# Optimization experiments

Hardware: AMD Instinct MI355X
Metric: run time of the kernel (lower is better)

Reference implementation:

```python
import jax, jax.numpy as jnp
import numpy as np

N = 100000   # nodes
E = 1600000  # edges (avg degree 16)
D = 64       # feature dim
STEPS = 3

def setup_inputs() -> dict:
    key = jax.random.key(0)
    ks = jax.random.split(key, 16)
    def rn(i, shape, scale=1.0):
        return jax.random.normal(ks[i], shape, dtype=jnp.float32) * scale
    inp = {
        "nodes": rn(0, (N, D)),
        "edges": rn(1, (E, D)),
        "globals_": rn(2, (1, D)),
        "senders": jax.random.randint(ks[3], (E,), 0, N, dtype=jnp.int32),
        "receivers": jax.random.randint(ks[4], (E,), 0, N, dtype=jnp.int32),
        # edge MLP: in 4*D -> D -> D
        "We1": rn(5, (4 * D, D), (4 * D) ** -0.5),
        "be1": jnp.zeros((D,), jnp.float32),
        "We2": rn(6, (D, D), D ** -0.5),
        "be2": jnp.zeros((D,), jnp.float32),
        # node MLP: in 3*D -> D -> D
        "Wn1": rn(7, (3 * D, D), (3 * D) ** -0.5),
        "bn1": jnp.zeros((D,), jnp.float32),
        "Wn2": rn(8, (D, D), D ** -0.5),
        "bn2": jnp.zeros((D,), jnp.float32),
        # global MLP: in 3*D -> D -> D
        "Wg1": rn(9, (3 * D, D), (3 * D) ** -0.5),
        "bg1": jnp.zeros((D,), jnp.float32),
        "Wg2": rn(10, (D, D), D ** -0.5),
        "bg2": jnp.zeros((D,), jnp.float32),
    }
    return inp

def _mlp(x, W1, b1, W2, b2):
    return jax.nn.relu(x @ W1 + b1) @ W2 + b2

def reference(nodes, edges, globals_, senders, receivers,
              We1, be1, We2, be2, Wn1, bn1, Wn2, bn2, Wg1, bg1, Wg2, bg2):
    g = globals_  # [1, D], single graph
    n_nodes = nodes.shape[0]
    for _ in range(STEPS):
        # --- edge update: gather sender/receiver node feats + broadcast globals ---
        sent = nodes[senders]        # [E, D]
        recv = nodes[receivers]      # [E, D]
        ge = jnp.broadcast_to(g, (edges.shape[0], g.shape[-1]))
        edges = _mlp(jnp.concatenate([edges, sent, recv, ge], axis=-1),
                     We1, be1, We2, be2)  # [E, D]
        # --- aggregate edges to nodes (received messages) ---
        received = jax.ops.segment_sum(edges, receivers, num_segments=n_nodes)
        gn = jnp.broadcast_to(g, (n_nodes, g.shape[-1]))
        nodes = _mlp(jnp.concatenate([nodes, received, gn], axis=-1),
                     Wn1, bn1, Wn2, bn2)  # [N, D]
        # --- aggregate to globals (single graph => full sums) ---
        agg_n = jnp.sum(nodes, axis=0, keepdims=True)  # [1, D]
        agg_e = jnp.sum(edges, axis=0, keepdims=True)  # [1, D]
        g = _mlp(jnp.concatenate([agg_n, agg_e, g], axis=-1),
                 Wg1, bg1, Wg2, bg2)  # [1, D]
    return nodes, edges, g
```

## Files before the change

kernel.cpp:

```cpp
#include <hip/hip_runtime.h>

#define DD 64
typedef unsigned int uint32;
typedef unsigned short ushort16;
typedef short bf16x8 __attribute__((ext_vector_type(8)));
typedef float f32x4 __attribute__((ext_vector_type(4)));
typedef uint32 u32x4 __attribute__((ext_vector_type(4)));

__device__ __forceinline__ ushort16 f2bf(float x) {
    uint32 u = __float_as_uint(x);
    uint32 r = (u + 0x7FFFu + ((u >> 16) & 1u)) >> 16;
    return (ushort16)r;
}
__device__ __forceinline__ float bf2f(ushort16 h) {
    return __uint_as_float(((uint32)h) << 16);
}

__device__ __forceinline__ void split8f(const float4& a, const float4& b, bf16x8& ah, bf16x8& al) {
    float xs[8] = {a.x, a.y, a.z, a.w, b.x, b.y, b.z, b.w};
#pragma unroll
    for (int i = 0; i < 8; ++i) {
        ushort16 hi = f2bf(xs[i]);
        ah[i] = (short)hi;
        al[i] = (short)f2bf(xs[i] - bf2f(hi));
    }
}

__device__ __forceinline__ void mfma_ks(const unsigned short* __restrict__ wks, int l,
                                        const bf16x8* ah, const bf16x8* al, f32x4 (*acc)[4]) {
#pragma unroll
    for (int tt = 0; tt < 4; ++tt) {
        bf16x8 bh = *(const bf16x8*)(wks + ((size_t)(tt * 2 + 0) * 64 + l) * 8);
        bf16x8 bl = *(const bf16x8*)(wks + ((size_t)(tt * 2 + 1) * 64 + l) * 8);
#pragma unroll
        for (int m = 0; m < 4; ++m) {
            acc[m][tt] = __builtin_amdgcn_mfma_f32_16x16x32_bf16(ah[m], bh, acc[m][tt], 0, 0, 0);
            acc[m][tt] = __builtin_amdgcn_mfma_f32_16x16x32_bf16(ah[m], bl, acc[m][tt], 0, 0, 0);
            acc[m][tt] = __builtin_amdgcn_mfma_f32_16x16x32_bf16(al[m], bh, acc[m][tt], 0, 0, 0);
        }
    }
}
__device__ __forceinline__ void mfma_ks_hi(const unsigned short* __restrict__ wks, int l,
                                           const bf16x8* ah, f32x4 (*acc)[4]) {
#pragma unroll
    for (int tt = 0; tt < 4; ++tt) {
        bf16x8 bh = *(const bf16x8*)(wks + ((size_t)(tt * 2 + 0) * 64 + l) * 8);
        bf16x8 bl = *(const bf16x8*)(wks + ((size_t)(tt * 2 + 1) * 64 + l) * 8);
#pragma unroll
        for (int m = 0; m < 4; ++m) {
            acc[m][tt] = __builtin_amdgcn_mfma_f32_16x16x32_bf16(ah[m], bh, acc[m][tt], 0, 0, 0);
            acc[m][tt] = __builtin_amdgcn_mfma_f32_16x16x32_bf16(ah[m], bl, acc[m][tt], 0, 0, 0);
        }
    }
}
__device__ __forceinline__ void mfma_ks1(const unsigned short* __restrict__ wks, int l,
                                         bf16x8 ah, bf16x8 al, f32x4* acc) {
#pragma unroll
    for (int tt = 0; tt < 4; ++tt) {
        bf16x8 bh = *(const bf16x8*)(wks + ((size_t)(tt * 2 + 0) * 64 + l) * 8);
        bf16x8 bl = *(const bf16x8*)(wks + ((size_t)(tt * 2 + 1) * 64 + l) * 8);
        acc[tt] = __builtin_amdgcn_mfma_f32_16x16x32_bf16(ah, bh, acc[tt], 0, 0, 0);
        acc[tt] = __builtin_amdgcn_mfma_f32_16x16x32_bf16(ah, bl, acc[tt], 0, 0, 0);
        acc[tt] = __builtin_amdgcn_mfma_f32_16x16x32_bf16(al, bh, acc[tt], 0, 0, 0);
    }
}
__device__ __forceinline__ void mfma_ks1_hi(const unsigned short* __restrict__ wks, int l,
                                            bf16x8 ah, f32x4* acc) {
#pragma unroll
    for (int tt = 0; tt < 4; ++tt) {
        bf16x8 bh = *(const bf16x8*)(wks + ((size_t)(tt * 2 + 0) * 64 + l) * 8);
        bf16x8 bl = *(const bf16x8*)(wks + ((size_t)(tt * 2 + 1) * 64 + l) * 8);
        acc[tt] = __builtin_amdgcn_mfma_f32_16x16x32_bf16(ah, bh, acc[tt], 0, 0, 0);
        acc[tt] = __builtin_amdgcn_mfma_f32_16x16x32_bf16(ah, bl, acc[tt], 0, 0, 0);
    }
}

__global__ void zero_counts_kernel(int* __restrict__ counts, int N) {
    int i = blockIdx.x * blockDim.x + threadIdx.x;
    if (i < N) counts[i] = 0;
}
__global__ void hist_kernel(const int* __restrict__ idx, int* __restrict__ counts, int E) {
    int i = blockIdx.x * blockDim.x + threadIdx.x;
    if (i < E) atomicAdd(&counts[idx[i]], 1);
}
__global__ __launch_bounds__(1024) void scan_kernel(const int* __restrict__ counts,
                                                    int* __restrict__ offs,
                                                    int* __restrict__ cursor, int N) {
    __shared__ int sm[1024];
    __shared__ int carryS;
    int t = threadIdx.x;
    if (t == 0) carryS = 0;
    __syncthreads();
    for (int base = 0; base < N; base += 4096) {
        int idx = base + t * 4;
        int x0 = (idx + 0 < N) ? counts[idx + 0] : 0;
        int x1 = (idx + 1 < N) ? counts[idx + 1] : 0;
        int x2 = (idx + 2 < N) ? counts[idx + 2] : 0;
        int x3 = (idx + 3 < N) ? counts[idx + 3] : 0;
        int s1 = x0 + x1, s2 = s1 + x2, s3 = s2 + x3;
        sm[t] = s3;
        __syncthreads();
        for (int d = 1; d < 1024; d <<= 1) {
            int v = (t >= d) ? sm[t - d] : 0;
            __syncthreads();
            sm[t] += v;
            __syncthreads();
        }
        int excl = sm[t] - s3 + carryS;
        if (idx < N)     { offs[idx]     = excl;      cursor[idx]     = excl; }
        if (idx + 1 < N) { offs[idx + 1] = excl + x0; cursor[idx + 1] = excl + x0; }
        if (idx + 2 < N) { offs[idx + 2] = excl + s1; cursor[idx + 2] = excl + s1; }
        if (idx + 3 < N) { offs[idx + 3] = excl + s2; cursor[idx + 3] = excl + s2; }
        int chunkTotal = sm[1023];
        __syncthreads();
        if (t == 0) carryS += chunkTotal;
        __syncthreads();
    }
    if (t == 0) offs[N] = carryS;
}
__global__ void scatter_kernel(const int* __restrict__ recv, int* __restrict__ cursor,
                               int* __restrict__ perm, int* __restrict__ inv, int E) {
    int i = blockIdx.x * blockDim.x + threadIdx.x;
    if (i < E) {
        int p = atomicAdd(&cursor[recv[i]], 1);
        perm[p] = i;
        inv[i] = p;
    }
}
__global__ void idxperm_kernel(const int* __restrict__ recv, const int* __restrict__ send,
                               const int* __restrict__ perm,
                               int* __restrict__ ridp, int* __restrict__ sidp, int E) {
    int i = blockIdx.x * blockDim.x + threadIdx.x;
    if (i < E) {
        int pe = perm[i];
        ridp[i] = recv[pe];
        sidp[i] = send[pe];
    }
}

__global__ void prep_bias_kernel(const float* __restrict__ g,
                                 const float* __restrict__ We1, const float* __restrict__ be1,
                                 const float* __restrict__ Wn1, const float* __restrict__ bn1,
                                 float* __restrict__ be1e, float* __restrict__ bn1e) {
    int j = threadIdx.x;
    float a = be1[j];
    float b = bn1[j];
    for (int k = 0; k < DD; ++k) {
        float gk = g[k];
        a = fmaf(gk, We1[(192 + k) * DD + j], a);
        b = fmaf(gk, Wn1[(128 + k) * DD + j], b);
    }
    be1e[j] = a;
    bn1e[j] = b;
}

__global__ void prep_nodes_kernel(const float* __restrict__ src,
                                  unsigned short* __restrict__ h, unsigned short* __restrict__ l,
                                  int total) {
    int i = blockIdx.x * blockDim.x + threadIdx.x;
    if (i < total) {
        float x = src[i];
        ushort16 hi = f2bf(x);
        h[i] = hi;
        l[i] = f2bf(x - bf2f(hi));
    }
}

__global__ void prep_edges_kernel(const float* __restrict__ e0, const int* __restrict__ inv,
                                  unsigned short* __restrict__ ebf, int E) {
    int tid = blockIdx.x * blockDim.x + threadIdx.x;
    if (tid < E * 8) {
        int e = tid >> 3, part = tid & 7;
        const float* p = e0 + (size_t)e * DD + part * 8;
        float4 a = *(const float4*)(p);
        float4 b = *(const float4*)(p + 4);
        u32x4 o;
        o.x = (uint32)f2bf(a.x) | ((uint32)f2bf(a.y) << 16);
        o.y = (uint32)f2bf(a.z) | ((uint32)f2bf(a.w) << 16);
        o.z = (uint32)f2bf(b.x) | ((uint32)f2bf(b.y) << 16);
        o.w = (uint32)f2bf(b.z) | ((uint32)f2bf(b.w) << 16);
        int ip = inv[e];
        *(u32x4*)(ebf + (size_t)ip * DD + part * 8) = o;
    }
}

__device__ __forceinline__ void prep_pack(const float* __restrict__ W, int nks,
                                          unsigned short* __restrict__ dst, int tid) {
    if (tid < nks * 2048) {
        int i = tid & 7, lane = (tid >> 3) & 63, tt = (tid >> 9) & 3, ks = tid >> 11;
        int k = ks * 32 + (lane >> 4) * 8 + i;
        int n = tt * 16 + (lane & 15);
        float x = W[k * DD + n];
        ushort16 hi = f2bf(x);
        ushort16 lo = f2bf(x - bf2f(hi));
        dst[(((ks * 4 + tt) * 2 + 0) * 64 + lane) * 8 + i] = hi;
        dst[(((ks * 4 + tt) * 2 + 1) * 64 + lane) * 8 + i] = lo;
    }
}
__global__ void prep_weights_kernel(const float* __restrict__ We1, const float* __restrict__ We2,
                                    const float* __restrict__ Wn1, const float* __restrict__ Wn2,
                                    unsigned short* __restrict__ we1p, unsigned short* __restrict__ we2p,
                                    unsigned short* __restrict__ wn1p, unsigned short* __restrict__ wn2p) {
    int tid = blockIdx.x * blockDim.x + threadIdx.x;
    prep_pack(We1, 6, we1p, tid);
    prep_pack(We2, 2, we2p, tid);
    prep_pack(Wn1, 4, wn1p, tid);
    prep_pack(Wn2, 2, wn2p, tid);
}

template<int IN_BF, int OUT_F32>
__global__ __launch_bounds__(256, 3) void edge_kernel_t(
    const float* __restrict__ edges_f32, const unsigned short* __restrict__ edges_bf,
    const unsigned short* __restrict__ nodes_h,
    const int* __restrict__ senders, const int* __restrict__ receivers,
    const int* __restrict__ ridp, const int* __restrict__ sidp,
    const int* __restrict__ perm,
    const unsigned short* __restrict__ w1, const float* __restrict__ b1,
    const unsigned short* __restrict__ w2, const float* __restrict__ b2,
    float* __restrict__ eout_f32, unsigned short* __restrict__ eout_bf,
    float* __restrict__ received, float* __restrict__ agg_e, int E)
{
    __shared__ int RID[4][64];
    __shared__ int PE[4][64];
    __shared__ float PS[4][64];
    __shared__ __align__(16) char HB[4][4096];

    const int t = threadIdx.x;
    const int w = t >> 6, l = t & 63;
    const int lm = l & 15, kq = l >> 4;
    const int base = (blockIdx.x << 8) + (w << 6);

    {
        int pos = min(base + l, E - 1);
        if (IN_BF) {
            RID[w][l] = ridp[pos];
            if (OUT_F32) PE[w][l] = perm[pos];
        } else {
            int pe = perm[pos];
            PE[w][l] = pe;
            RID[w][l] = receivers[pe];
        }
    }

    int ridPrevWave, ridNextWave;
    {
        int pb = base - 1;
        int nb2 = base + 64;
        if (IN_BF) {
            ridPrevWave = (pb >= 0) ? ridp[pb] : -1;
            ridNextWave = (nb2 < E) ? ridp[nb2] : -1;
        } else {
            ridPrevWave = (pb >= 0) ? receivers[perm[pb]] : -1;
            ridNextWave = (nb2 < E) ? receivers[perm[nb2]] : -1;
        }
    }

    int sid_m[4];
#pragma unroll
    for (int m = 0; m < 4; ++m) {
        int pos = min(base + (m << 4) + lm, E - 1);
        if (IN_BF) sid_m[m] = sidp[pos];
    }
    int pe_m[4];
    int rid_m[4];
#pragma unroll
    for (int m = 0; m < 4; ++m) {
        rid_m[m] = RID[w][(m << 4) + lm];
        if (OUT_F32 || !IN_BF) pe_m[m] = PE[w][(m << 4) + lm];
        if (!IN_BF) sid_m[m] = senders[pe_m[m]];
    }

    u32x4 rbe[4][2];
    float4 re[4][4];
    if (IN_BF) {
#pragma unroll
        for (int m = 0; m < 4; ++m) {
            int row = min(base + (m << 4) + lm, E - 1);
            const unsigned short* p = edges_bf + (size_t)row * DD + kq * 8;
            rbe[m][0] = __builtin_nontemporal_load((const u32x4*)(p));
            rbe[m][1] = __builtin_nontemporal_load((const u32x4*)(p + 32));
        }
    } else {
#pragma unroll
        for (int m = 0; m < 4; ++m) {
            const float* p = edges_f32 + (size_t)pe_m[m] * DD + kq * 8;
            re[m][0] = *(const float4*)(p);
            re[m][1] = *(const float4*)(p + 4);
            re[m][2] = *(const float4*)(p + 32);
            re[m][3] = *(const float4*)(p + 36);
        }
    }
    uint4 rsh[4][2];
#pragma unroll
    for (int m = 0; m < 4; ++m) {
        const unsigned short* p = nodes_h + (size_t)sid_m[m] * DD + kq * 8;
        rsh[m][0] = *(const uint4*)(p);
        rsh[m][1] = *(const uint4*)(p + 32);
    }
    uint4 rrh[4][2];
#pragma unroll
    for (int m = 0; m < 4; ++m) {
        const unsigned short* ph = nodes_h + (size_t)rid_m[m] * DD + kq * 8;
        rrh[m][0] = *(const uint4*)(ph);
        rrh[m][1] = *(const uint4*)(ph + 32);
    }

    f32x4 acc[4][4];
#pragma unroll
    for (int tt = 0; tt < 4; ++tt) {
        float b = b1[tt * 16 + lm];
#pragma unroll
        for (int m = 0; m < 4; ++m) { acc[m][tt][0] = b; acc[m][tt][1] = b; acc[m][tt][2] = b; acc[m][tt][3] = b; }
    }

    if (IN_BF) {
#pragma unroll
        for (int ks2 = 0; ks2 < 2; ++ks2) {
            bf16x8 ah[4];
#pragma unroll
            for (int m = 0; m < 4; ++m) ah[m] = *(bf16x8*)&rbe[m][ks2];
            mfma_ks_hi(w1 + (size_t)ks2 * 4096, l, ah, acc);
        }
    } else {
#pragma unroll
        for (int ks2 = 0; ks2 < 2; ++ks2) {
            bf16x8 ah[4], al[4];
#pragma unroll
            for (int m = 0; m < 4; ++m) split8f(re[m][ks2 * 2], re[m][ks2 * 2 + 1], ah[m], al[m]);
            mfma_ks(w1 + (size_t)ks2 * 4096, l, ah, al, acc);
        }
    }
#pragma unroll
    for (int ks2 = 0; ks2 < 2; ++ks2) {
        bf16x8 ah[4];
#pragma unroll
        for (int m = 0; m < 4; ++m) ah[m] = *(bf16x8*)&rsh[m][ks2];
        mfma_ks_hi(w1 + (size_t)(2 + ks2) * 4096, l, ah, acc);
    }
#pragma unroll
    for (int ks2 = 0; ks2 < 2; ++ks2) {
        bf16x8 ah[4];
#pragma unroll
        for (int m = 0; m < 4; ++m) ah[m] = *(bf16x8*)&rrh[m][ks2];
        mfma_ks_hi(w1 + (size_t)(4 + ks2) * 4096, l, ah, acc);
    }

    float b2v[4];
#pragma unroll
    for (int tt = 0; tt < 4; ++tt) b2v[tt] = b2[tt * 16 + lm];
    float sreg[4] = {0.f, 0.f, 0.f, 0.f};
    float run = 0.f;
    bool firstFlush = true;
    char* hh = &HB[w][0];

#pragma unroll
    for (int m = 0; m < 4; ++m) {
#pragma unroll
        for (int tt = 0; tt < 4; ++tt)
#pragma unroll
            for (int r = 0; r < 4; ++r) {
                int row = (kq << 2) + r;
                int col = (tt << 4) + lm;
                float hv = fmaxf(acc[m][tt][r], 0.f);
                int boff = (row << 7) + ((((col >> 3) ^ (row & 7)) & 7) << 4) + ((col & 7) << 1);
                *(unsigned short*)(hh + boff) = f2bf(hv);
            }

        f32x4 acc2[4];
#pragma unroll
        for (int tt = 0; tt < 4; ++tt) { acc2[tt][0] = b2v[tt]; acc2[tt][1] = b2v[tt]; acc2[tt][2] = b2v[tt]; acc2[tt][3] = b2v[tt]; }
#pragma unroll
        for (int ks = 0; ks < 2; ++ks) {
            int boff = (lm << 7) + ((((kq + ks * 4) ^ (lm & 7)) & 7) << 4);
            bf16x8 ah = *(const bf16x8*)(hh + boff);
            mfma_ks1_hi(w2 + (size_t)ks * 4096, l, ah, acc2);
        }

#pragma unroll
        for (int tt = 0; tt < 4; ++tt)
#pragma unroll
            for (int r = 0; r < 4; ++r) {
                int rowp = base + (m << 4) + (kq << 2) + r;
                if (rowp < E) sreg[tt] += acc2[tt][r];
            }

#pragma unroll
        for (int tt = 0; tt < 4; ++tt)
#pragma unroll
            for (int r = 0; r < 4; ++r) {
                int row = (kq << 2) + r;
                int col = (tt << 4) + lm;
                int boff = (row << 8) + ((((col >> 2) ^ (row & 15)) & 15) << 4) + ((col & 3) << 2);
                *(float*)(&HB[w][0] + boff) = acc2[tt][r];
            }

        {
            int rowp = base + (m << 4) + lm;
            f32x4 vv[4];
#pragma unroll
            for (int jj = 0; jj < 4; ++jj) {
                int slot = (4 * kq + jj) ^ (lm & 15);
                vv[jj] = *(f32x4*)(&HB[w][0] + (lm << 8) + (slot << 4));
            }
            if (rowp < E) {
                if (OUT_F32) {
                    f32x4* dst = (f32x4*)(eout_f32 + (size_t)pe_m[m] * DD);
#pragma unroll
                    for (int jj = 0; jj < 4; ++jj) dst[kq * 4 + jj] = vv[jj];
                } else {
                    u32x4 o0, o1;
                    o0.x = (uint32)f2bf(vv[0][0]) | ((uint32)f2bf(vv[0][1]) << 16);
                    o0.y = (uint32)f2bf(vv[0][2]) | ((uint32)f2bf(vv[0][3]) << 16);
                    o0.z = (uint32)f2bf(vv[1][0]) | ((uint32)f2bf(vv[1][1]) << 16);
                    o0.w = (uint32)f2bf(vv[1][2]) | ((uint32)f2bf(vv[1][3]) << 16);
                    o1.x = (uint32)f2bf(vv[2][0]) | ((uint32)f2bf(vv[2][1]) << 16);
                    o1.y = (uint32)f2bf(vv[2][2]) | ((uint32)f2bf(vv[2][3]) << 16);
                    o1.z = (uint32)f2bf(vv[3][0]) | ((uint32)f2bf(vv[3][1]) << 16);
                    o1.w = (uint32)f2bf(vv[3][2]) | ((uint32)f2bf(vv[3][3]) << 16);
                    unsigned short* dst = eout_bf + (size_t)rowp * DD + kq * 16;
                    *(u32x4*)(dst) = o0;
                    *(u32x4*)(dst + 8) = o1;
                }
            }
        }

        {
#pragma unroll
            for (int r = 0; r < 16; ++r) {
                int wr = (m << 4) + r;
                int rowp = base + wr;
                if (rowp < E) {
                    int boff = (r << 8) + ((((l >> 2) ^ (r & 15)) & 15) << 4) + ((l & 3) << 2);
                    float v = *(const float*)(&HB[w][0] + boff);
                    int rid = RID[w][wr];
                    run += v;
                    bool flush;
                    if (wr == 63) flush = true;
                    else flush = (rowp + 1 >= E) || (RID[w][wr + 1] != rid);
                    if (flush) {
                        bool shared_seg = (firstFlush && rid == ridPrevWave) ||
                                          ((wr == 63) && (rowp + 1 < E) && rid == ridNextWave);
                        float* dst = &received[(size_t)rid * DD + l];
                        if (shared_seg) atomicAdd(dst, run);
                        else *dst = run;
                        run = 0.f;
                        firstFlush = false;
                    }
                }
            }
        }
    }

#pragma unroll
    for (int tt = 0; tt < 4; ++tt) {
        float s = sreg[tt];
        s += __shfl_xor(s, 16, 64);
        s += __shfl_xor(s, 32, 64);
        if (l < 16) PS[w][tt * 16 + l] = s;
    }
    __syncthreads();
    if (t < 64) {
        float s = PS[0][t] + PS[1][t] + PS[2][t] + PS[3][t];
        atomicAdd(agg_e + t, s);
    }
}

__global__ __launch_bounds__(256, 2) void node_kernel_mfma(
    const unsigned short* __restrict__ nodes_h_in, const unsigned short* __restrict__ nodes_l_in,
    const float* __restrict__ received,
    const unsigned short* __restrict__ w1, const float* __restrict__ b1,
    const unsigned short* __restrict__ w2, const float* __restrict__ b2,
    float* __restrict__ nodes_out,
    unsigned short* __restrict__ nodes_h_out, unsigned short* __restrict__ nodes_l_out,
    int write_pk, float* __restrict__ agg_n, int N)
{
    __shared__ unsigned short HB[4][4][2][1024];
    __shared__ float PS[4][64];

    const int t = threadIdx.x;
    const int w = t >> 6, l = t & 63;
    const int lm = l & 15, kq = l >> 4;
    const int base = (blockIdx.x << 8) + (w << 6);

    int gi[4];
#pragma unroll
    for (int m = 0; m < 4; ++m) gi[m] = min(base + (m << 4) + lm, N - 1);

    uint4 rnh[4][2], rnl[4][2];
#pragma unroll
    for (int m = 0; m < 4; ++m) {
        const unsigned short* ph = nodes_h_in + (size_t)gi[m] * DD + kq * 8;
        const unsigned short* pl = nodes_l_in + (size_t)gi[m] * DD + kq * 8;
        rnh[m][0] = *(const uint4*)(ph);
        rnh[m][1] = *(const uint4*)(ph + 32);
        rnl[m][0] = *(const uint4*)(pl);
        rnl[m][1] = *(const uint4*)(pl + 32);
    }
    float4 rc[4][4];
#pragma unroll
    for (int m = 0; m < 4; ++m) {
        const float* p = received + (size_t)gi[m] * DD + kq * 8;
        rc[m][0] = *(const float4*)(p);
        rc[m][1] = *(const float4*)(p + 4);
        rc[m][2] = *(const float4*)(p + 32);
        rc[m][3] = *(const float4*)(p + 36);
    }

    f32x4 acc[4][4];
#pragma unroll
    for (int tt = 0; tt < 4; ++tt) {
        float b = b1[tt * 16 + lm];
#pragma unroll
        for (int m = 0; m < 4; ++m) { acc[m][tt][0] = b; acc[m][tt][1] = b; acc[m][tt][2] = b; acc[m][tt][3] = b; }
    }

#pragma unroll
    for (int ks2 = 0; ks2 < 2; ++ks2) {
        bf16x8 ah[4], al[4];
#pragma unroll
        for (int m = 0; m < 4; ++m) { ah[m] = *(bf16x8*)&rnh[m][ks2]; al[m] = *(bf16x8*)&rnl[m][ks2]; }
        mfma_ks(w1 + (size_t)ks2 * 4096, l, ah, al, acc);
    }
#pragma unroll
    for (int ks2 = 0; ks2 < 2; ++ks2) {
        bf16x8 ah[4], al[4];
#pragma unroll
        for (int m = 0; m < 4; ++m) split8f(rc[m][ks2 * 2], rc[m][ks2 * 2 + 1], ah[m], al[m]);
        mfma_ks(w1 + (size_t)(2 + ks2) * 4096, l, ah, al, acc);
    }

#pragma unroll
    for (int m = 0; m < 4; ++m) {
        char* hh = (char*)&HB[w][m][0][0];
        char* hl = (char*)&HB[w][m][1][0];
#pragma unroll
        for (int tt = 0; tt < 4; ++tt)
#pragma unroll
            for (int r = 0; r < 4; ++r) {
                int row = (kq << 2) + r;
                int col = (tt << 4) + lm;
                float hv = fmaxf(acc[m][tt][r], 0.f);
                ushort16 hi = f2bf(hv);
                ushort16 lo = f2bf(hv - bf2f(hi));
                int boff = (row << 7) + ((((col >> 3) ^ (row & 7)) & 7) << 4) + ((col & 7) << 1);
                *(unsigned short*)(hh + boff) = hi;
                *(unsigned short*)(hl + boff) = lo;
            }
    }

    f32x4 acc2[4][4];
#pragma unroll
    for (int tt = 0; tt < 4; ++tt) {
        float b = b2[tt * 16 + lm];
#pragma unroll
        for (int m = 0; m < 4; ++m) { acc2[m][tt][0] = b; acc2[m][tt][1] = b; acc2[m][tt][2] = b; acc2[m][tt][3] = b; }
    }
#pragma unroll
    for (int ks = 0; ks < 2; ++ks) {
        bf16x8 ah[4], al[4];
#pragma unroll
        for (int m = 0; m < 4; ++m) {
            int boff = (lm << 7) + ((((kq + ks * 4) ^ (lm & 7)) & 7) << 4);
            ah[m] = *(const bf16x8*)((char*)&HB[w][m][0][0] + boff);
            al[m] = *(const bf16x8*)((char*)&HB[w][m][1][0] + boff);
        }
        mfma_ks(w2 + (size_t)ks * 4096, l, ah, al, acc2);
    }

#pragma unroll
    for (int tt = 0; tt < 4; ++tt) {
        float s = 0.f;
#pragma unroll
        for (int m = 0; m < 4; ++m)
#pragma unroll
            for (int r = 0; r < 4; ++r) {
                int rowg = base + (m << 4) + (kq << 2) + r;
                if (rowg < N) s += acc2[m][tt][r];
            }
        s += __shfl_xor(s, 16, 64);
        s += __shfl_xor(s, 32, 64);
        if (l < 16) PS[w][tt * 16 + l] = s;
    }

    char* CW = (char*)&HB[w][0][0][0];
#pragma unroll
    for (int m = 0; m < 4; ++m)
#pragma unroll
        for (int tt = 0; tt < 4; ++tt)
#pragma unroll
            for (int r = 0; r < 4; ++r) {
                int row = (kq << 2) + r;
                int col = (tt << 4) + lm;
                int boff = (row << 8) + ((((col >> 2) ^ (row & 15)) & 15) << 4) + ((col & 3) << 2);
                *(float*)(CW + m * 4096 + boff) = acc2[m][tt][r];
            }
#pragma unroll
    for (int m = 0; m < 4; ++m) {
        int rowg = base + (m << 4) + lm;
        float4 vv[4];
#pragma unroll
        for (int jj = 0; jj < 4; ++jj) {
            int slot = (4 * kq + jj) ^ (lm & 15);
            vv[jj] = *(float4*)(CW + m * 4096 + (lm << 8) + (slot << 4));
        }
        if (rowg < N) {
            float4* dst = (float4*)(nodes_out + (size_t)rowg * DD);
#pragma unroll
            for (int jj = 0; jj < 4; ++jj) dst[kq * 4 + jj] = vv[jj];
            if (write_pk) {
                unsigned short* hdst = nodes_h_out + (size_t)rowg * DD + kq * 16;
                unsigned short* ldst = nodes_l_out + (size_t)rowg * DD + kq * 16;
                uint4 oh, ol;
                float xs[16] = {vv[0].x, vv[0].y, vv[0].z, vv[0].w,
                                vv[1].x, vv[1].y, vv[1].z, vv[1].w,
                                vv[2].x, vv[2].y, vv[2].z, vv[2].w,
                                vv[3].x, vv[3].y, vv[3].z, vv[3].w};
                uint32 hw[8], lw[8];
#pragma unroll
                for (int q = 0; q < 8; ++q) {
                    ushort16 h0 = f2bf(xs[2 * q]);
                    ushort16 h1 = f2bf(xs[2 * q + 1]);
                    ushort16 l0 = f2bf(xs[2 * q] - bf2f(h0));
                    ushort16 l1 = f2bf(xs[2 * q + 1] - bf2f(h1));
                    hw[q] = (uint32)h0 | ((uint32)h1 << 16);
                    lw[q] = (uint32)l0 | ((uint32)l1 << 16);
                }
                oh.x = hw[0]; oh.y = hw[1]; oh.z = hw[2]; oh.w = hw[3];
                *(uint4*)(hdst) = oh;
                oh.x = hw[4]; oh.y = hw[5]; oh.z = hw[6]; oh.w = hw[7];
                *(uint4*)(hdst + 8) = oh;
                ol.x = lw[0]; ol.y = lw[1]; ol.z = lw[2]; ol.w = lw[3];
                *(uint4*)(ldst) = ol;
                ol.x = lw[4]; ol.y = lw[5]; ol.z = lw[6]; ol.w = lw[7];
                *(uint4*)(ldst + 8) = ol;
            }
        }
    }

    __syncthreads();
    if (t < 64) {
        float s = PS[0][t] + PS[1][t] + PS[2][t] + PS[3][t];
        atomicAdd(agg_n + t, s);
    }
}

__global__ void global_kernel(const float* __restrict__ agg_n, const float* __restrict__ agg_e,
                              const float* __restrict__ g_in,
                              const float* __restrict__ Wg1, const float* __restrict__ bg1,
                              const float* __restrict__ Wg2, const float* __restrict__ bg2,
                              float* __restrict__ g_out)
{
    __shared__ float h[64];
    int j = threadIdx.x;
    float a = bg1[j];
    for (int k = 0; k < DD; ++k) a = fmaf(agg_n[k], Wg1[k * DD + j], a);
    for (int k = 0; k < DD; ++k) a = fmaf(agg_e[k], Wg1[(64 + k) * DD + j], a);
    for (int k = 0; k < DD; ++k) a = fmaf(g_in[k],  Wg1[(128 + k) * DD + j], a);
    h[j] = fmaxf(a, 0.f);
    __syncthreads();
    float o = bg2[j];
    for (int k = 0; k < DD; ++k) o = fmaf(h[k], Wg2[k * DD + j], o);
    g_out[j] = o;
}

extern "C" void kernel_launch(void* const* d_in, const int* in_sizes, int n_in,
                              void* d_out, int out_size, void* d_ws, size_t ws_size,
                              hipStream_t stream) {
    const float* nodes0 = (const float*)d_in[0];
    const float* edges0 = (const float*)d_in[1];
    const float* g0     = (const float*)d_in[2];
    const int* senders   = (const int*)d_in[3];
    const int* receivers = (const int*)d_in[4];
    const float* We1 = (const float*)d_in[5];
    const float* be1 = (const float*)d_in[6];
    const float* We2 = (const float*)d_in[7];
    const float* be2 = (const float*)d_in[8];
    const float* Wn1 = (const float*)d_in[9];
    const float* bn1 = (const float*)d_in[10];
    const float* Wn2 = (const float*)d_in[11];
    const float* bn2 = (const float*)d_in[12];
    const float* Wg1 = (const float*)d_in[13];
    const float* bg1 = (const float*)d_in[14];
    const float* Wg2 = (const float*)d_in[15];
    const float* bg2 = (const float*)d_in[16];

    const int N = in_sizes[0] / DD;
    const int E = in_sizes[1] / DD;

    float* out_nodes = (float*)d_out;
    float* out_edges = out_nodes + (size_t)N * DD;
    float* out_g     = out_edges + (size_t)E * DD;

    float* ws = (float*)d_ws;
    float* received = ws;
    float* aggs = received + (size_t)N * DD;
    float* agg_n = aggs;
    float* agg_e = aggs + 64;
    float* b1e   = aggs + 128;
    float* b1n   = aggs + 192;
    float* g1    = aggs + 256;
    float* g2    = aggs + 320;
    int* counts = (int*)(aggs + 512);
    int* offs   = counts + N;
    int* cursor = offs + N + 4;
    int* perm   = cursor + N;
    int* inv    = perm + E;
    int* ridp   = inv + E;
    int* sidp   = ridp + E;
    unsigned short* nodes_h = (unsigned short*)(sidp + E);
    unsigned short* nodes_l = nodes_h + (size_t)N * DD;
    unsigned short* we1p = nodes_l + (size_t)N * DD;
    unsigned short* we2p = we1p + 24576;
    unsigned short* wn1p = we2p + 8192;
    unsigned short* wn2p = wn1p + 16384;
    unsigned short* edges_bf = wn2p + 8192;

    size_t need_bf = (size_t)((char*)(edges_bf + (size_t)E * DD) - (char*)d_ws);
    const bool use_bf = (ws_size >= need_bf);

    const int eblocks = (E + 255) / 256;
    const int nblocks = (N + 255) / 256;

    zero_counts_kernel<<<(N + 255) / 256, 256, 0, stream>>>(counts, N);
    hist_kernel<<<(E + 255) / 256, 256, 0, stream>>>(receivers, counts, E);
    scan_kernel<<<1, 1024, 0, stream>>>(counts, offs, cursor, N);
    scatter_kernel<<<(E + 255) / 256, 256, 0, stream>>>(receivers, cursor, perm, inv, E);
    prep_weights_kernel<<<48, 256, 0, stream>>>(We1, We2, Wn1, Wn2, we1p, we2p, wn1p, wn2p);
    prep_nodes_kernel<<<(N * DD + 255) / 256, 256, 0, stream>>>(nodes0, nodes_h, nodes_l, N * DD);
    if (use_bf) {
        idxperm_kernel<<<(E + 255) / 256, 256, 0, stream>>>(receivers, senders, perm, ridp, sidp, E);
        prep_edges_kernel<<<(E * 8 + 255) / 256, 256, 0, stream>>>(edges0, inv, edges_bf, E);
    }

    for (int s = 0; s < 3; ++s) {
        const float* esrc_f32 = (s == 0) ? edges0 : out_edges;
        const float* gin  = (s == 0) ? g0 : ((s == 1) ? g1 : g2);
        float* gout       = (s == 2) ? out_g : ((s == 0) ? g1 : g2);

        hipMemsetAsync(received, 0, ((size_t)N * DD + 128) * sizeof(float), stream);
        prep_bias_kernel<<<1, 64, 0, stream>>>(gin, We1, be1, Wn1, bn1, b1e, b1n);

        if (use_bf) {
            if (s == 2)
                edge_kernel_t<1, 1><<<eblocks, 256, 0, stream>>>(esrc_f32, edges_bf, nodes_h,
                    senders, receivers, ridp, sidp, perm, we1p, b1e, we2p, be2,
                    out_edges, edges_bf, received, agg_e, E);
            else
                edge_kernel_t<1, 0><<<eblocks, 256, 0, stream>>>(esrc_f32, edges_bf, nodes_h,
                    senders, receivers, ridp, sidp, perm, we1p, b1e, we2p, be2,
                    out_edges, edges_bf, received, agg_e, E);
        } else {
            edge_kernel_t<0, 1><<<eblocks, 256, 0, stream>>>(esrc_f32, edges_bf, nodes_h,
                senders, receivers, ridp, sidp, perm, we1p, b1e, we2p, be2,
                out_edges, edges_bf, received, agg_e, E);
        }

        node_kernel_mfma<<<nblocks, 256, 0, stream>>>(nodes_h, nodes_l, received,
                                                      wn1p, b1n, wn2p, bn2,
                                                      out_nodes, nodes_h, nodes_l,
                                                      (s < 2) ? 1 : 0, agg_n, N);
        global_kernel<<<1, 64, 0, stream>>>(agg_n, agg_e, gin, Wg1, bg1, Wg2, bg2, gout);
    }
}
```

Before: 1.948 ms.

## Halve node-kernel rows per wave and stream second layer per row tile

The node MLP kernel now processes 32 rows per wave (128 per block) instead of 64, cutting register arrays and raising launch bounds to 3 blocks per CU. The second layer, reduction and output are restructured to run per 16-row tile, reusing a smaller shared buffer (16KB instead of 64KB). This aims to raise occupancy and reduce LDS pressure in the node update, at the cost of more blocks and repeated weight loads per row.

Measured after the change: 1.949 ms. About the same (+0.1%).

```diff
diff --git a/kernel.cpp b/kernel.cpp
--- a/kernel.cpp
+++ b/kernel.cpp
@@ -26,28 +26,30 @@
     }
 }
 
-__device__ __forceinline__ void mfma_ks(const unsigned short* __restrict__ wks, int l,
-                                        const bf16x8* ah, const bf16x8* al, f32x4 (*acc)[4]) {
+template<int M>
+__device__ __forceinline__ void mfma_ksT(const unsigned short* __restrict__ wks, int l,
+                                         const bf16x8* ah, const bf16x8* al, f32x4 (*acc)[4]) {
 #pragma unroll
     for (int tt = 0; tt < 4; ++tt) {
         bf16x8 bh = *(const bf16x8*)(wks + ((size_t)(tt * 2 + 0) * 64 + l) * 8);
         bf16x8 bl = *(const bf16x8*)(wks + ((size_t)(tt * 2 + 1) * 64 + l) * 8);
 #pragma unroll
-        for (int m = 0; m < 4; ++m) {
+        for (int m = 0; m < M; ++m) {
             acc[m][tt] = __builtin_amdgcn_mfma_f32_16x16x32_bf16(ah[m], bh, acc[m][tt], 0, 0, 0);
             acc[m][tt] = __builtin_amdgcn_mfma_f32_16x16x32_bf16(ah[m], bl, acc[m][tt], 0, 0, 0);
             acc[m][tt] = __builtin_amdgcn_mfma_f32_16x16x32_bf16(al[m], bh, acc[m][tt], 0, 0, 0);
         }
     }
 }
-__device__ __forceinline__ void mfma_ks_hi(const unsigned short* __restrict__ wks, int l,
-                                           const bf16x8* ah, f32x4 (*acc)[4]) {
+template<int M>
+__device__ __forceinline__ void mfma_ksT_hi(const unsigned short* __restrict__ wks, int l,
+                                            const bf16x8* ah, f32x4 (*acc)[4]) {
 #pragma unroll
     for (int tt = 0; tt < 4; ++tt) {
         bf16x8 bh = *(const bf16x8*)(wks + ((size_t)(tt * 2 + 0) * 64 + l) * 8);
         bf16x8 bl = *(const bf16x8*)(wks + ((size_t)(tt * 2 + 1) * 64 + l) * 8);
 #pragma unroll
-        for (int m = 0; m < 4; ++m) {
+        for (int m = 0; m < M; ++m) {
             acc[m][tt] = __builtin_amdgcn_mfma_f32_16x16x32_bf16(ah[m], bh, acc[m][tt], 0, 0, 0);
             acc[m][tt] = __builtin_amdgcn_mfma_f32_16x16x32_bf16(ah[m], bl, acc[m][tt], 0, 0, 0);
         }
@@ -319,7 +321,7 @@
             bf16x8 ah[4];
 #pragma unroll
             for (int m = 0; m < 4; ++m) ah[m] = *(bf16x8*)&rbe[m][ks2];
-            mfma_ks_hi(w1 + (size_t)ks2 * 4096, l, ah, acc);
+            mfma_ksT_hi<4>(w1 + (size_t)ks2 * 4096, l, ah, acc);
         }
     } else {
 #pragma unroll
@@ -327,7 +329,7 @@
             bf16x8 ah[4], al[4];
 #pragma unroll
             for (int m = 0; m < 4; ++m) split8f(re[m][ks2 * 2], re[m][ks2 * 2 + 1], ah[m], al[m]);
-            mfma_ks(w1 + (size_t)ks2 * 4096, l, ah, al, acc);
+            mfma_ksT<4>(w1 + (size_t)ks2 * 4096, l, ah, al, acc);
         }
     }
 #pragma unroll
@@ -335,14 +337,14 @@
         bf16x8 ah[4];
 #pragma unroll
         for (int m = 0; m < 4; ++m) ah[m] = *(bf16x8*)&rsh[m][ks2];
-        mfma_ks_hi(w1 + (size_t)(2 + ks2) * 4096, l, ah, acc);
+        mfma_ksT_hi<4>(w1 + (size_t)(2 + ks2) * 4096, l, ah, acc);
     }
 #pragma unroll
     for (int ks2 = 0; ks2 < 2; ++ks2) {
         bf16x8 ah[4];
 #pragma unroll
         for (int m = 0; m < 4; ++m) ah[m] = *(bf16x8*)&rrh[m][ks2];
-        mfma_ks_hi(w1 + (size_t)(4 + ks2) * 4096, l, ah, acc);
+        mfma_ksT_hi<4>(w1 + (size_t)(4 + ks2) * 4096, l, ah, acc);
     }
 
     float b2v[4];
@@ -465,7 +467,7 @@
     }
 }
 
-__global__ __launch_bounds__(256, 2) void node_kernel_mfma(
+__global__ __launch_bounds__(256, 3) void node_kernel_mfma(
     const unsigned short* __restrict__ nodes_h_in, const unsigned short* __restrict__ nodes_l_in,
     const float* __restrict__ received,
     const unsigned short* __restrict__ w1, const float* __restrict__ b1,
@@ -474,21 +476,21 @@
     unsigned short* __restrict__ nodes_h_out, unsigned short* __restrict__ nodes_l_out,
     int write_pk, float* __restrict__ agg_n, int N)
 {
-    __shared__ unsigned short HB[4][4][2][1024];
+    __shared__ __align__(16) char HB[4][4096];
     __shared__ float PS[4][64];
 
     const int t = threadIdx.x;
     const int w = t >> 6, l = t & 63;
     const int lm = l & 15, kq = l >> 4;
-    const int base = (blockIdx.x << 8) + (w << 6);
-
-    int gi[4];
-#pragma unroll
-    for (int m = 0; m < 4; ++m) gi[m] = min(base + (m << 4) + lm, N - 1);
-
-    uint4 rnh[4][2], rnl[4][2];
-#pragma unroll
-    for (int m = 0; m < 4; ++m) {
+    const int base = (blockIdx.x << 7) + (w << 5);
+
+    int gi[2];
+#pragma unroll
+    for (int m = 0; m < 2; ++m) gi[m] = min(base + (m << 4) + lm, N - 1);
+
+    uint4 rnh[2][2], rnl[2][2];
+#pragma unroll
+    for (int m = 0; m < 2; ++m) {
         const unsigned short* ph = nodes_h_in + (size_t)gi[m] * DD + kq * 8;
         const unsigned short* pl = nodes_l_in + (size_t)gi[m] * DD + kq * 8;
         rnh[m][0] = *(const uint4*)(ph);
@@ -496,9 +498,9 @@
         rnl[m][0] = *(const uint4*)(pl);
         rnl[m][1] = *(const uint4*)(pl + 32);
     }
-    float4 rc[4][4];
-#pragma unroll
-    for (int m = 0; m < 4; ++m) {
+    float4 rc[2][4];
+#pragma unroll
+    for (int m = 0; m < 2; ++m) {
         const float* p = received + (size_t)gi[m] * DD + kq * 8;
         rc[m][0] = *(const float4*)(p);
         rc[m][1] = *(const float4*)(p + 4);
@@ -506,33 +508,38 @@
         rc[m][3] = *(const float4*)(p + 36);
     }
 
-    f32x4 acc[4][4];
+    f32x4 acc[2][4];
 #pragma unroll
     for (int tt = 0; tt < 4; ++tt) {
         float b = b1[tt * 16 + lm];
 #pragma unroll
-        for (int m = 0; m < 4; ++m) { acc[m][tt][0] = b; acc[m][tt][1] = b; acc[m][tt][2] = b; acc[m][tt][3] = b; }
+        for (int m = 0; m < 2; ++m) { acc[m][tt][0] = b; acc[m][tt][1] = b; acc[m][tt][2] = b; acc[m][tt][3] = b; }
     }
 
 #pragma unroll
     for (int ks2 = 0; ks2 < 2; ++ks2) {
-        bf16x8 ah[4], al[4];
-#pragma unroll
-        for (int m = 0; m < 4; ++m) { ah[m] = *(bf16x8*)&rnh[m][ks2]; al[m] = *(bf16x8*)&rnl[m][ks2]; }
-        mfma_ks(w1 + (size_t)ks2 * 4096, l, ah, al, acc);
+        bf16x8 ah[2], al[2];
+#pragma unroll
+        for (int m = 0; m < 2; ++m) { ah[m] = *(bf16x8*)&rnh[m][ks2]; al[m] = *(bf16x8*)&rnl[m][ks2]; }
+        mfma_ksT<2>(w1 + (size_t)ks2 * 4096, l, ah, al, acc);
     }
 #pragma unroll
     for (int ks2 = 0; ks2 < 2; ++ks2) {
-        bf16x8 ah[4], al[4];
-#pragma unroll
-        for (int m = 0; m < 4; ++m) split8f(rc[m][ks2 * 2], rc[m][ks2 * 2 + 1], ah[m], al[m]);
-        mfma_ks(w1 + (size_t)(2 + ks2) * 4096, l, ah, al, acc);
-    }
-
-#pragma unroll
-    for (int m = 0; m < 4; ++m) {
-        char* hh = (char*)&HB[w][m][0][0];
-        char* hl = (char*)&HB[w][m][1][0];
+        bf16x8 ah[2], al[2];
+#pragma unroll
+        for (int m = 0; m < 2; ++m) split8f(rc[m][ks2 * 2], rc[m][ks2 * 2 + 1], ah[m], al[m]);
+        mfma_ksT<2>(w1 + (size_t)(2 + ks2) * 4096, l, ah, al, acc);
+    }
+
+    float b2v[4];
+#pragma unroll
+    for (int tt = 0; tt < 4; ++tt) b2v[tt] = b2[tt * 16 + lm];
+    float sreg[4] = {0.f, 0.f, 0.f, 0.f};
+    char* hh = &HB[w][0];
+    char* hl = &HB[w][2048];
+
+#pragma unroll
+    for (int m = 0; m < 2; ++m) {
 #pragma unroll
         for (int tt = 0; tt < 4; ++tt)
 #pragma unroll
@@ -546,45 +553,26 @@
                 *(unsigned short*)(hh + boff) = hi;
                 *(unsigned short*)(hl + boff) = lo;
             }
-    }
-
-    f32x4 acc2[4][4];
-#pragma unroll
-    for (int tt = 0; tt < 4; ++tt) {
-        float b = b2[tt * 16 + lm];
-#pragma unroll
-        for (int m = 0; m < 4; ++m) { acc2[m][tt][0] = b; acc2[m][tt][1] = b; acc2[m][tt][2] = b; acc2[m][tt][3] = b; }
-    }
-#pragma unroll
-    for (int ks = 0; ks < 2; ++ks) {
-        bf16x8 ah[4], al[4];
-#pragma unroll
-        for (int m = 0; m < 4; ++m) {
+
+        f32x4 acc2[4];
+#pragma unroll
+        for (int tt = 0; tt < 4; ++tt) { acc2[tt][0] = b2v[tt]; acc2[tt][1] = b2v[tt]; acc2[tt][2] = b2v[tt]; acc2[tt][3] = b2v[tt]; }
+#pragma unroll
+        for (int ks = 0; ks < 2; ++ks) {
             int boff = (lm << 7) + ((((kq + ks * 4) ^ (lm & 7)) & 7) << 4);
-            ah[m] = *(const bf16x8*)((char*)&HB[w][m][0][0] + boff);
-            al[m] = *(const bf16x8*)((char*)&HB[w][m][1][0] + boff);
-        }
-        mfma_ks(w2 + (size_t)ks * 4096, l, ah, al, acc2);
-    }
-
-#pragma unroll
-    for (int tt = 0; tt < 4; ++tt) {
-        float s = 0.f;
-#pragma unroll
-        for (int m = 0; m < 4; ++m)
+            bf16x8 ah = *(const bf16x8*)(hh + boff);
+            bf16x8 al = *(const bf16x8*)(hl + boff);
+            mfma_ks1(w2 + (size_t)ks * 4096, l, ah, al, acc2);
+        }
+
+#pragma unroll
+        for (int tt = 0; tt < 4; ++tt)
 #pragma unroll
             for (int r = 0; r < 4; ++r) {
                 int rowg = base + (m << 4) + (kq << 2) + r;
-                if (rowg < N) s += acc2[m][tt][r];
-            }
-        s += __shfl_xor(s, 16, 64);
-        s += __shfl_xor(s, 32, 64);
-        if (l < 16) PS[w][tt * 16 + l] = s;
-    }
-
-    char* CW = (char*)&HB[w][0][0][0];
-#pragma unroll
-    for (int m = 0; m < 4; ++m)
+                if (rowg < N) sreg[tt] += acc2[tt][r];
+            }
+
 #pragma unroll
         for (int tt = 0; tt < 4; ++tt)
 #pragma unroll
@@ -592,51 +580,59 @@
                 int row = (kq << 2) + r;
                 int col = (tt << 4) + lm;
                 int boff = (row << 8) + ((((col >> 2) ^ (row & 15)) & 15) << 4) + ((col & 3) << 2);
-                *(float*)(CW + m * 4096 + boff) = acc2[m][tt][r];
-            }
-#pragma unroll
-    for (int m = 0; m < 4; ++m) {
-        int rowg = base + (m << 4) + lm;
-        float4 vv[4];
-#pragma unroll
-        for (int jj = 0; jj < 4; ++jj) {
-            int slot = (4 * kq + jj) ^ (lm & 15);
-            vv[jj] = *(float4*)(CW + m * 4096 + (lm << 8) + (slot << 4));
-        }
-        if (rowg < N) {
-            float4* dst = (float4*)(nodes_out + (size_t)rowg * DD);
-#pragma unroll
-            for (int jj = 0; jj < 4; ++jj) dst[kq * 4 + jj] = vv[jj];
-            if (write_pk) {
-                unsigned short* hdst = nodes_h_out + (size_t)rowg * DD + kq * 16;
-                unsigned short* ldst = nodes_l_out + (size_t)rowg * DD + kq * 16;
-                uint4 oh, ol;
-                float xs[16] = {vv[0].x, vv[0].y, vv[0].z, vv[0].w,
-                                vv[1].x, vv[1].y, vv[1].z, vv[1].w,
-                                vv[2].x, vv[2].y, vv[2].z, vv[2].w,
-                                vv[3].x, vv[3].y, vv[3].z, vv[3].w};
-                uint32 hw[8], lw[8];
-#pragma unroll
-                for (int q = 0; q < 8; ++q) {
-                    ushort16 h0 = f2bf(xs[2 * q]);
-                    ushort16 h1 = f2bf(xs[2 * q + 1]);
-                    ushort16 l0 = f2bf(xs[2 * q] - bf2f(h0));
-                    ushort16 l1 = f2bf(xs[2 * q + 1] - bf2f(h1));
-                    hw[q] = (uint32)h0 | ((uint32)h1 << 16);
-                    lw[q] = (uint32)l0 | ((uint32)l1 << 16);
+                *(float*)(&HB[w][0] + boff) = acc2[tt][r];
+            }
+
+        {
+            int rowg = base + (m << 4) + lm;
+            float4 vv[4];
+#pragma unroll
+            for (int jj = 0; jj < 4; ++jj) {
+                int slot = (4 * kq + jj) ^ (lm & 15);
+                vv[jj] = *(float4*)(&HB[w][0] + (lm << 8) + (slot << 4));
+            }
+            if (rowg < N) {
+                float4* dst = (float4*)(nodes_out + (size_t)rowg * DD);
+#pragma unroll
+                for (int jj = 0; jj < 4; ++jj) dst[kq * 4 + jj] = vv[jj];
+                if (write_pk) {
+                    unsigned short* hdst = nodes_h_out + (size_t)rowg * DD + kq * 16;
+                    unsigned short* ldst = nodes_l_out + (size_t)rowg * DD + kq * 16;
+                    float xs[16] = {vv[0].x, vv[0].y, vv[0].z, vv[0].w,
+                                    vv[1].x, vv[1].y, vv[1].z, vv[1].w,
+                                    vv[2].x, vv[2].y, vv[2].z, vv[2].w,
+                                    vv[3].x, vv[3].y, vv[3].z, vv[3].w};
+                    uint32 hw[8], lw[8];
+#pragma unroll
+                    for (int q = 0; q < 8; ++q) {
+                        ushort16 h0 = f2bf(xs[2 * q]);
+                        ushort16 h1 = f2bf(xs[2 * q + 1]);
+                        ushort16 l0 = f2bf(xs[2 * q] - bf2f(h0));
+                        ushort16 l1 = f2bf(xs[2 * q + 1] - bf2f(h1));
+                        hw[q] = (uint32)h0 | ((uint32)h1 << 16);
+                        lw[q] = (uint32)l0 | ((uint32)l1 << 16);
+                    }
+                    uint4 oh, ol;
+                    oh.x = hw[0]; oh.y = hw[1]; oh.z = hw[2]; oh.w = hw[3];
+                    *(uint4*)(hdst) = oh;
+                    oh.x = hw[4]; oh.y = hw[5]; oh.z = hw[6]; oh.w = hw[7];
+                    *(uint4*)(hdst + 8) = oh;
+                    ol.x = lw[0]; ol.y = lw[1]; ol.z = lw[2]; ol.w = lw[3];
+                    *(uint4*)(ldst) = ol;
+                    ol.x = lw[4]; ol.y = lw[5]; ol.z = lw[6]; ol.w = lw[7];
+                    *(uint4*)(ldst + 8) = ol;
                 }
-                oh.x = hw[0]; oh.y = hw[1]; oh.z = hw[2]; oh.w = hw[3];
-                *(uint4*)(hdst) = oh;
-                oh.x = hw[4]; oh.y = hw[5]; oh.z = hw[6]; oh.w = hw[7];
-                *(uint4*)(hdst + 8) = oh;
-                ol.x = lw[0]; ol.y = lw[1]; ol.z = lw[2]; ol.w = lw[3];
-                *(uint4*)(ldst) = ol;
-                ol.x = lw[4]; ol.y = lw[5]; ol.z = lw[6]; ol.w = lw[7];
-                *(uint4*)(ldst + 8) = ol;
-            }
-        }
-    }
-
+            }
+        }
+    }
+
+#pragma unroll
+    for (int tt = 0; tt < 4; ++tt) {
+        float s = sreg[tt];
+        s += __shfl_xor(s, 16, 64);
+        s += __shfl_xor(s, 32, 64);
+        if (l < 16) PS[w][tt * 16 + l] = s;
+    }
     __syncthreads();
     if (t < 64) {
         float s = PS[0][t] + PS[1][t] + PS[2][t] + PS[3][t];
@@ -719,7 +715,7 @@
     const bool use_bf = (ws_size >= need_bf);
 
     const int eblocks = (E + 255) / 256;
-    const int nblocks = (N + 255) / 256;
+    const int nblocks = (N + 127) / 128;
 
     zero_counts_kernel<<<(N + 255) / 256, 256, 0, stream>>>(counts, N);
     hist_kernel<<<(E + 255) / 256, 256, 0, stream>>>(receivers, counts, E);
```
